# Kernel tuning notes

Hardware: AMD Instinct MI355X
Metric: run time of the kernel (lower is better)

The kernel has to match this reference:

```python
import jax, jax.numpy as jnp
import numpy as np

B, RES, NS, W, S = 2, 64, 24, 256, 256
IN_VIEW = W + 3


def setup_inputs() -> dict:
    key = jax.random.key(0)
    ks = iter(jax.random.split(key, 32))
    u = lambda k, shape, a: jax.random.uniform(k, shape, jnp.float32, -a, a)
    c_hid = float(np.sqrt(6.0 / W) / 25.0)      # SIREN hidden init bound
    c_view = float(np.sqrt(6.0 / IN_VIEW) / 25.0)
    inp = {}
    # camera: identity rotation, camera at z=1 looking down -z (StyleSDF-like)
    pose = np.zeros((B, 3, 4), np.float32)
    pose[:, 0, 0] = 1.0; pose[:, 1, 1] = 1.0; pose[:, 2, 2] = 1.0; pose[:, 2, 3] = 1.0
    inp['cam_poses'] = jnp.asarray(pose)
    inp['focal'] = jnp.full((B, 1, 1), 87.0, jnp.float32)
    inp['near'] = jnp.full((B, 1, 1), 0.88, jnp.float32)
    inp['far'] = jnp.full((B, 1, 1), 1.12, jnp.float32)
    inp['styles'] = jax.random.normal(next(ks), (B, S), jnp.float32)
    # FiLM-SIREN point layers
    inp['w0'] = u(next(ks), (W, 3), 1.0 / 3.0)
    inp['b0'] = u(next(ks), (W,), float(np.sqrt(1.0 / 3.0)))
    inp['ws'] = u(next(ks), (7, W, W), c_hid)
    inp['bs'] = u(next(ks), (7, W), float(np.sqrt(1.0 / W)))
    inp['gamma_w'] = 0.02 * jax.random.normal(next(ks), (8, W, S), jnp.float32)
    inp['gamma_b'] = u(next(ks), (8, W), float(np.sqrt(1.0 / S)))
    inp['beta_w'] = 0.02 * jax.random.normal(next(ks), (8, W, S), jnp.float32)
    inp['beta_b'] = u(next(ks), (8, W), float(np.sqrt(1.0 / S)))
    # view-conditioned FiLM layer
    inp['view_w'] = u(next(ks), (W, IN_VIEW), c_view)
    inp['view_b'] = u(next(ks), (W,), float(np.sqrt(1.0 / IN_VIEW)))
    inp['view_gw'] = 0.02 * jax.random.normal(next(ks), (W, S), jnp.float32)
    inp['view_gb'] = u(next(ks), (W,), float(np.sqrt(1.0 / S)))
    inp['view_bw'] = 0.02 * jax.random.normal(next(ks), (W, S), jnp.float32)
    inp['view_bb'] = u(next(ks), (W,), float(np.sqrt(1.0 / S)))
    # output heads (freq_init)
    inp['rgb_w'] = u(next(ks), (3, W), c_hid)
    inp['rgb_b'] = u(next(ks), (3,), float(np.sqrt(1.0 / W)))
    inp['sigma_w'] = u(next(ks), (1, W), c_hid)
    inp['sigma_b'] = u(next(ks), (1,), float(np.sqrt(1.0 / W)))
    inp['sigmoid_beta'] = 0.1 * jnp.ones((1,), jnp.float32)
    return inp


def _film(x, style, w, b, gw, gb, bw, bb):
    # x: [B,h,w,n,in] ; FiLM-SIREN: sin(gamma * (xW^T + b) + beta)
    out = jnp.einsum('bhwni,oi->bhwno', x, w) + b
    gamma = 15.0 * (style @ gw.T + gb) + 30.0          # LinearLayer(std=15, bias_init=30)
    beta = 0.25 * (style @ bw.T + bb)                  # LinearLayer(std=0.25, bias_init=0)
    return jnp.sin(gamma[:, None, None, None, :] * out + beta[:, None, None, None, :])


def _forward(cam_poses, focal, near, far, styles, w0, b0, ws, bs, gamma_w, gamma_b,
             beta_w, beta_b, view_w, view_b, view_gw, view_gb, view_bw, view_bb,
             rgb_w, rgb_b, sigma_w, sigma_b, sigmoid_beta):
    b = cam_poses.shape[0]
    # --- get_rays (buffers i, j from meshgrid, transposed) ---
    lin = jnp.linspace(0.5, RES - 0.5, RES)
    ii = jnp.broadcast_to(lin[None, :], (RES, RES))[None]  # varies along width
    jj = jnp.broadcast_to(lin[:, None], (RES, RES))[None]  # varies along height
    dirs = jnp.stack([
        jnp.broadcast_to((ii - RES * 0.5) / focal, (b, RES, RES)),
        jnp.broadcast_to(-(jj - RES * 0.5) / focal, (b, RES, RES)),
        -jnp.ones((b, RES, RES), focal.dtype)], -1)        # [B,h,w,3]
    rays_d = jnp.einsum('bhwc,bkc->bhwk', dirs, cam_poses[:, :3, :3])
    rays_o = jnp.broadcast_to(cam_poses[:, None, None, :3, -1], rays_d.shape)
    viewdirs = rays_d / jnp.linalg.norm(rays_d, axis=-1, keepdims=True)
    # --- render_rays (test: perturb=0) ---
    near4 = near[..., None] * jnp.ones_like(rays_d[..., :1])   # [B,h,w,1]
    far4 = far[..., None] * jnp.ones_like(rays_d[..., :1])
    t_vals = jnp.linspace(0.0, 1.0 - 1.0 / NS, NS)             # offset_sampling
    z_vals = near4 * (1.0 - t_vals) + far4 * t_vals            # [B,h,w,NS]
    pts = rays_o[..., None, :] + rays_d[..., None, :] * z_vals[..., None]  # [B,h,w,NS,3]
    norm_pts = pts * (2.0 / (far4 - near4))[..., None, :]      # z_normalize
    # --- SirenGenerator (styles.ndim==2 path, no hyper deltas) ---
    h = _film(norm_pts, styles, w0, b0, gamma_w[0], gamma_b[0], beta_w[0], beta_b[0])
    for i in range(7):
        h = _film(h, styles, ws[i], bs[i], gamma_w[i + 1], gamma_b[i + 1],
                  beta_w[i + 1], beta_b[i + 1])
    sdf = jnp.einsum('bhwni,oi->bhwno', h, sigma_w) + sigma_b  # [B,h,w,NS,1]
    dirs_exp = jnp.broadcast_to(viewdirs[..., None, :], pts.shape)
    h = jnp.concatenate([h, dirs_exp], -1)                     # [B,h,w,NS,W+3]
    feat = _film(h, styles, view_w, view_b, view_gw, view_gb, view_bw, view_bb)
    rgb = jnp.einsum('bhwni,oi->bhwno', feat, rgb_w) + rgb_b   # [B,h,w,NS,3]
    # --- volume_integration (with_sdf, test: no noise) ---
    rays_d_norm = jnp.linalg.norm(rays_d, axis=-1, keepdims=True)        # [B,h,w,1]
    dists = jnp.concatenate([z_vals[..., 1:] - z_vals[..., :-1],
                             jnp.full_like(rays_d_norm, 1e10)], -1)      # [B,h,w,NS]
    dists = dists * rays_d_norm
    sigma = jax.nn.sigmoid(-sdf / sigmoid_beta) / sigmoid_beta
    alpha = 1.0 - jnp.exp(-sigma * dists[..., None])                      # [B,h,w,NS,1]
    ones = jnp.ones_like(alpha[..., :1, :])
    vis = jnp.cumprod(jnp.concatenate([ones, 1.0 - alpha + 1e-10], 3), 3)[..., :-1, :]
    weights = alpha * vis
    # force_background: last sample absorbs the remaining transmittance
    bg = 1.0 - jnp.sum(weights[..., :-1, :], axis=3)
    weights = jnp.concatenate([weights[..., :-1, :], bg[..., None, :]], 3)
    rgb_map = -1.0 + 2.0 * jnp.sum(weights * jax.nn.sigmoid(rgb), axis=3)  # [B,h,w,3]
    feature_map = jnp.sum(weights * feat, axis=3)                          # [B,h,w,W]
    return jnp.concatenate([rgb_map, feature_map], -1)                     # [B,h,w,3+W]


def reference(cam_poses, focal, near, far, styles, w0, b0, ws, bs, gamma_w, gamma_b,
              beta_w, beta_b, view_w, view_b, view_gw, view_gb, view_bw, view_bb,
              rgb_w, rgb_b, sigma_w, sigma_b, sigmoid_beta):
    return _forward(cam_poses, focal, near, far, styles, w0, b0, ws, bs, gamma_w,
                    gamma_b, beta_w, beta_b, view_w, view_b, view_gw, view_gb,
                    view_bw, view_bb, rgb_w, rgb_b, sigma_w, sigma_b, sigmoid_beta)
```

## Files before the change

### kernel.cpp

```cpp
#include <hip/hip_runtime.h>
#include <hip/hip_bf16.h>

#define RESN 64
#define NS 24
#define WD 256
#define SD 256
#define NB 2
#define RPB 4
#define MP 96
#define NTH 512
#define NBLK 2048

typedef unsigned short u16;
typedef unsigned int u32;
typedef __attribute__((ext_vector_type(8))) short short8v;
typedef __attribute__((ext_vector_type(16))) float f32x16;

__device__ __forceinline__ float sigm(float x){ return 1.0f / (1.0f + expf(-x)); }

__device__ __forceinline__ float fast_sin(float x){
  float k = __builtin_rintf(x * 0.31830988618f);
  float y = fmaf(k, -3.14159274101f, x);
  y = fmaf(k, 8.74227766e-8f, y);
  float y2 = y * y;
  float p = fmaf(y2, 2.75573192e-6f, -1.98412698e-4f);
  p = fmaf(y2, p, 8.33333333e-3f);
  p = fmaf(y2, p, -1.66666667e-1f);
  float s = fmaf(y * y2, p, y);
  u32 sg = ((u32)((int)k) & 1u) << 31;
  return __uint_as_float(__float_as_uint(s) ^ sg);
}

__global__ void prep_kernel(const float* wsp, const float* vw, u16* Whi, u16* Wlo){
  int i0 = (blockIdx.x * 256 + threadIdx.x) * 4;
  #pragma unroll
  for (int j = 0; j < 4; j++){
    int e = i0 + j;
    int lay = e >> 16;
    int rk = e & 65535;
    float w = (lay < 7) ? wsp[lay * 65536 + rk]
                        : vw[(size_t)(rk >> 8) * 259 + (rk & 255)];
    u32 b = __float_as_uint(w);
    u16 hi = (u16)(b >> 16);
    float lof = w - __uint_as_float(b & 0xFFFF0000u);
    Whi[e] = hi;
    Wlo[e] = (u16)(__float_as_uint(lof) >> 16);
  }
}

__global__ void film_kernel(const float* styles, const float* gw8, const float* gb8,
                            const float* bw8, const float* bb8,
                            const float* vgw, const float* vgb, const float* vbw, const float* vbb,
                            float* G, float* Bt){
  int l = blockIdx.x >> 1, b = blockIdx.x & 1, o = threadIdx.x;
  __shared__ float st[SD];
  st[o] = styles[b * SD + o];
  __syncthreads();
  const float *gw, *bw; float gbv, bbv;
  if (l < 8){
    gw = gw8 + ((size_t)l * WD + o) * SD; bw = bw8 + ((size_t)l * WD + o) * SD;
    gbv = gb8[l * WD + o];                bbv = bb8[l * WD + o];
  } else {
    gw = vgw + (size_t)o * SD;            bw = vbw + (size_t)o * SD;
    gbv = vgb[o];                         bbv = vbb[o];
  }
  float ag = 0.f, ab = 0.f;
  for (int s = 0; s < SD; s += 2){
    ag += st[s] * gw[s] + st[s+1] * gw[s+1];
    ab += st[s] * bw[s] + st[s+1] * bw[s+1];
  }
  int idx = (l * NB + b) * WD + o;
  G[idx]  = 15.0f * (ag + gbv) + 30.0f;
  Bt[idx] = 0.25f * (ab + bbv);
}

#define SETW(LAY) { wph = Whi + (((size_t)(LAY) * WD + col) * WD) + khalf * 8;   \
                    wpl = Wlo + (((size_t)(LAY) * WD + col) * WD) + khalf * 8; }

#define PREF4 { _Pragma("unroll")                                                \
  for (int i = 0; i < 4; i++){                                                   \
    pbh[i] = *(const short8v*)(wph + i * 16);                                    \
    pbl[i] = *(const short8v*)(wpl + i * 16); } }

#define KMAIN                                                                    \
  _Pragma("unroll")                                                              \
  for (int ks = 0; ks < 16; ks++){                                               \
    short8v bh = pbh[ks & 3], bl = pbl[ks & 3];                                  \
    if (ks < 12){ pbh[ks & 3] = *(const short8v*)(wph + (ks + 4) * 16);          \
                  pbl[ks & 3] = *(const short8v*)(wpl + (ks + 4) * 16); }        \
    int ce = 2 * ks + khalf;                                                     \
    _Pragma("unroll")                                                            \
    for (int mt = 0; mt < 3; mt++){                                              \
      int elem = (mt * 32 + lane31) * WD + ((ce ^ l7) * 8);                      \
      short8v ah = *(const short8v*)(&Hhi[elem]);                                \
      short8v al = *(const short8v*)(&Hlo[elem]);                                \
      acc[mt] = __builtin_amdgcn_mfma_f32_32x32x16_bf16(ah, bh, acc[mt], 0,0,0); \
      acc[mt] = __builtin_amdgcn_mfma_f32_32x32x16_bf16(al, bh, acc[mt], 0,0,0); \
      acc[mt] = __builtin_amdgcn_mfma_f32_32x32x16_bf16(ah, bl, acc[mt], 0,0,0); \
    } }

__launch_bounds__(NTH, 2)
__global__ void render_mfma(
    const float* pose, const float* focal, const float* nearv, const float* farv,
    const float* w0, const float* b0, const float* bsp,
    const float* vw, const float* vb,
    const float* rgbw, const float* rgbb, const float* sgw, const float* sgb,
    const float* sbeta, const float* G, const float* Bt,
    const u16* Whi, const u16* Wlo, float* out)
{
  __shared__ u16 Hhi[MP * WD];
  __shared__ u16 Hlo[MP * WD];
  __shared__ float xl[MP][4];
  __shared__ float vd[RPB][4];
  __shared__ float dn[RPB];
  __shared__ float sdfl[MP];
  __shared__ float rgbl[MP][4];
  __shared__ float wtl[RPB][NS];
  __shared__ float swl[WD];
  __shared__ float rwl[3][WD];

  const int t      = threadIdx.x;
  const int lane   = t & 63;
  const int wv     = t >> 6;
  const int lane31 = lane & 31;
  const int khalf  = lane >> 5;
  const int l7     = lane31 & 7;
  const int col    = wv * 32 + lane31;
  const int om     = t & 127;
  const int mg     = t >> 7;
  const int o0     = om * 2, o1 = om * 2 + 1;
  const int mb     = mg * NS;
  const int ray0   = blockIdx.x * RPB;
  const int bidx   = ray0 >> 12;

  const u16 *wph, *wpl;
  short8v pbh[4], pbl[4];
  SETW(0); PREF4;

  if (t < WD) swl[t] = sgw[t];
  for (int i = t; i < 3 * WD; i += NTH) ((float*)rwl)[i] = rgbw[i];

  if (t < MP){
    int m = t, s = m % NS, rl = m / NS;
    int ray = ray0 + rl;
    int ww = ray & (RESN - 1);
    int hh = (ray >> 6) & (RESN - 1);
    float f = focal[bidx], nr = nearv[bidx], fr = farv[bidx];
    float di = ((ww + 0.5f) - RESN * 0.5f) / f;
    float dj = -(((hh + 0.5f) - RESN * 0.5f) / f);
    const float* P = pose + bidx * 12;
    float rdx = di * P[0] + dj * P[1] - P[2];
    float rdy = di * P[4] + dj * P[5] - P[6];
    float rdz = di * P[8] + dj * P[9] - P[10];
    float ox = P[3], oy = P[7], oz = P[11];
    float nrm = sqrtf(rdx * rdx + rdy * rdy + rdz * rdz);
    const float C = (1.0f - 1.0f / NS) / (NS - 1);
    float tv = s * C;
    float z = nr * (1.0f - tv) + fr * tv;
    float sc = 2.0f / (fr - nr);
    xl[m][0] = (ox + rdx * z) * sc;
    xl[m][1] = (oy + rdy * z) * sc;
    xl[m][2] = (oz + rdz * z) * sc;
    if (s == 0){
      vd[rl][0] = rdx / nrm; vd[rl][1] = rdy / nrm; vd[rl][2] = rdz / nrm;
      dn[rl] = nrm;
    }
  }
  __syncthreads();

  {
    float wa[3], wbv[3];
    #pragma unroll
    for (int j = 0; j < 3; j++){ wa[j] = w0[o0 * 3 + j]; wbv[j] = w0[o1 * 3 + j]; }
    float bi0 = b0[o0], bi1 = b0[o1];
    float g0 = G[bidx * WD + o0],  g1 = G[bidx * WD + o1];
    float e0 = Bt[bidx * WD + o0], e1 = Bt[bidx * WD + o1];
    #pragma unroll
    for (int m = 0; m < NS; m++){
      int row = mb + m;
      float x0 = xl[row][0], x1 = xl[row][1], x2 = xl[row][2];
      float u0 = x0 * wa[0]  + x1 * wa[1]  + x2 * wa[2]  + bi0;
      float u1 = x0 * wbv[0] + x1 * wbv[1] + x2 * wbv[2] + bi1;
      float s0 = fast_sin(fmaf(g0, u0, e0));
      float s1 = fast_sin(fmaf(g1, u1, e1));
      u32 bs0 = __float_as_uint(s0), bs1 = __float_as_uint(s1);
      u32 hw = (bs0 >> 16) | (bs1 & 0xFFFF0000u);
      float l0f = s0 - __uint_as_float(bs0 & 0xFFFF0000u);
      float l1f = s1 - __uint_as_float(bs1 & 0xFFFF0000u);
      u32 lw = (__float_as_uint(l0f) >> 16) | (__float_as_uint(l1f) & 0xFFFF0000u);
      int eidx = row * WD + (((o0 >> 3) ^ (row & 7)) * 8) + (o0 & 7);
      *(u32*)&Hhi[eidx] = hw;
      *(u32*)&Hlo[eidx] = lw;
    }
  }
  __syncthreads();

  #pragma unroll 1
  for (int l = 0; l < 7; l++){
    f32x16 acc[3];
    #pragma unroll
    for (int mt = 0; mt < 3; mt++)
      #pragma unroll
      for (int j = 0; j < 16; j++) acc[mt][j] = 0.f;
    KMAIN
    float g  = G[((l + 1) * NB + bidx) * WD + col];
    float e  = Bt[((l + 1) * NB + bidx) * WD + col];
    float bi = bsp[l * WD + col];
    __syncthreads();
    #pragma unroll
    for (int mt = 0; mt < 3; mt++){
      #pragma unroll
      for (int rg = 0; rg < 16; rg++){
        int row = mt * 32 + (rg & 3) + 8 * (rg >> 2) + 4 * khalf;
        float a = acc[mt][rg] + bi;
        float s = fast_sin(fmaf(g, a, e));
        u32 sb = __float_as_uint(s);
        int eidx = row * WD + ((((col >> 3) ^ (row & 7))) * 8) + (col & 7);
        Hhi[eidx] = (u16)(sb >> 16);
        float sl = s - __uint_as_float(sb & 0xFFFF0000u);
        Hlo[eidx] = (u16)(__float_as_uint(sl) >> 16);
      }
    }
    SETW(l + 1); PREF4;
    __syncthreads();
  }

  f32x16 acc[3];
  #pragma unroll
  for (int mt = 0; mt < 3; mt++)
    #pragma unroll
    for (int j = 0; j < 16; j++) acc[mt][j] = 0.f;
  KMAIN
  float vt0 = vw[(size_t)col * 259 + 256];
  float vt1 = vw[(size_t)col * 259 + 257];
  float vt2 = vw[(size_t)col * 259 + 258];
  float vbv = vb[col];
  float gv = G[(8 * NB + bidx) * WD + col];
  float ev = Bt[(8 * NB + bidx) * WD + col];

  if (t < MP){
    float a = 0.f;
    #pragma unroll 4
    for (int c = 0; c < 32; c++){
      int eb = t * WD + ((c ^ (t & 7)) * 8);
      short8v hv = *(const short8v*)(&Hhi[eb]);
      short8v lv = *(const short8v*)(&Hlo[eb]);
      #pragma unroll
      for (int j = 0; j < 8; j++){
        float h = __uint_as_float(((u32)(u16)hv[j]) << 16)
                + __uint_as_float(((u32)(u16)lv[j]) << 16);
        a = fmaf(h, swl[c * 8 + j], a);
      }
    }
    sdfl[t] = a + sgb[0];
  }
  __syncthreads();

  #pragma unroll
  for (int mt = 0; mt < 3; mt++){
    #pragma unroll
    for (int rg = 0; rg < 16; rg++){
      int row = mt * 32 + (rg & 3) + 8 * (rg >> 2) + 4 * khalf;
      int ray = (row >= 48) ? ((row >= 72) ? 3 : 2) : ((row >= 24) ? 1 : 0);
      float c = vd[ray][0] * vt0 + vd[ray][1] * vt1 + vd[ray][2] * vt2 + vbv;
      float a = acc[mt][rg] + c;
      float s = fast_sin(fmaf(gv, a, ev));
      u32 sb = __float_as_uint(s);
      int eidx = row * WD + ((((col >> 3) ^ (row & 7))) * 8) + (col & 7);
      Hhi[eidx] = (u16)(sb >> 16);
      float sl = s - __uint_as_float(sb & 0xFFFF0000u);
      Hlo[eidx] = (u16)(__float_as_uint(sl) >> 16);
    }
  }
  __syncthreads();

  if (t < MP){
    float a0 = 0.f, a1 = 0.f, a2 = 0.f;
    #pragma unroll 4
    for (int c = 0; c < 32; c++){
      int eb = t * WD + ((c ^ (t & 7)) * 8);
      short8v hv = *(const short8v*)(&Hhi[eb]);
      short8v lv = *(const short8v*)(&Hlo[eb]);
      #pragma unroll
      for (int j = 0; j < 8; j++){
        float h = __uint_as_float(((u32)(u16)hv[j]) << 16)
                + __uint_as_float(((u32)(u16)lv[j]) << 16);
        int k = c * 8 + j;
        a0 = fmaf(h, rwl[0][k], a0);
        a1 = fmaf(h, rwl[1][k], a1);
        a2 = fmaf(h, rwl[2][k], a2);
      }
    }
    rgbl[t][0] = a0 + rgbb[0];
    rgbl[t][1] = a1 + rgbb[1];
    rgbl[t][2] = a2 + rgbb[2];
  }
  __syncthreads();

  if (t < RPB){
    int r = t;
    int ray = ray0 + r;
    float nr = nearv[bidx], fr = farv[bidx];
    float dnv = dn[r];
    float bet = sbeta[0];
    float vis = 1.f, wsum = 0.f, cr = 0.f, cg = 0.f, cb = 0.f;
    const float C = (1.0f - 1.0f / NS) / (NS - 1);
    #pragma unroll
    for (int s = 0; s < NS; s++){
      float w;
      if (s < NS - 1){
        float t0v = s * C, t1v = (s + 1) * C;
        float z0 = nr * (1.f - t0v) + fr * t0v;
        float z1 = nr * (1.f - t1v) + fr * t1v;
        float dist = (z1 - z0) * dnv;
        float sg = sigm(-sdfl[r * NS + s] / bet) / bet;
        float al = 1.f - expf(-sg * dist);
        w = al * vis;
        vis *= (1.f - al + 1e-10f);
        wsum += w;
      } else {
        w = 1.f - wsum;
      }
      wtl[r][s] = w;
      cr += w * sigm(rgbl[r * NS + s][0]);
      cg += w * sigm(rgbl[r * NS + s][1]);
      cb += w * sigm(rgbl[r * NS + s][2]);
    }
    size_t ob = (size_t)ray * 259;
    out[ob + 0] = -1.f + 2.f * cr;
    out[ob + 1] = -1.f + 2.f * cg;
    out[ob + 2] = -1.f + 2.f * cb;
  }
  __syncthreads();

  {
    float f0 = 0.f, f1 = 0.f;
    #pragma unroll
    for (int s = 0; s < NS; s++){
      int row = mb + s;
      float w = wtl[mg][s];
      int eidx = row * WD + (((o0 >> 3) ^ (row & 7)) * 8) + (o0 & 7);
      u32 wh = *(const u32*)&Hhi[eidx];
      u32 wl = *(const u32*)&Hlo[eidx];
      float fa = __uint_as_float(wh << 16) + __uint_as_float(wl << 16);
      float fb = __uint_as_float(wh & 0xFFFF0000u) + __uint_as_float(wl & 0xFFFF0000u);
      f0 = fmaf(w, fa, f0);
      f1 = fmaf(w, fb, f1);
    }
    size_t ob = (size_t)(ray0 + mg) * 259 + 3;
    out[ob + o0] = f0;
    out[ob + o1] = f1;
  }
}

extern "C" void kernel_launch(void* const* d_in, const int* in_sizes, int n_in,
                              void* d_out, int out_size, void* d_ws, size_t ws_size,
                              hipStream_t stream) {
  (void)in_sizes; (void)n_in; (void)out_size;
  const float* pose   = (const float*)d_in[0];
  const float* focal  = (const float*)d_in[1];
  const float* nearv  = (const float*)d_in[2];
  const float* farv   = (const float*)d_in[3];
  const float* styles = (const float*)d_in[4];
  const float* w0     = (const float*)d_in[5];
  const float* b0     = (const float*)d_in[6];
  const float* wsp    = (const float*)d_in[7];
  const float* bsp    = (const float*)d_in[8];
  const float* gw8    = (const float*)d_in[9];
  const float* gb8    = (const float*)d_in[10];
  const float* bw8    = (const float*)d_in[11];
  const float* bb8    = (const float*)d_in[12];
  const float* vw     = (const float*)d_in[13];
  const float* vb     = (const float*)d_in[14];
  const float* vgw    = (const float*)d_in[15];
  const float* vgb    = (const float*)d_in[16];
  const float* vbw    = (const float*)d_in[17];
  const float* vbb    = (const float*)d_in[18];
  const float* rgbw   = (const float*)d_in[19];
  const float* rgbb   = (const float*)d_in[20];
  const float* sgw    = (const float*)d_in[21];
  const float* sgb    = (const float*)d_in[22];
  const float* sbeta  = (const float*)d_in[23];

  float* G  = (float*)d_ws;
  float* Bt = G + 9 * NB * WD;
  float* out = (float*)d_out;

  const size_t plane_off = 36864;
  const size_t plane_elems = (size_t)8 * WD * WD;

  u16* Whi = (u16*)((char*)d_ws + plane_off);
  u16* Wlo = Whi + plane_elems;

  film_kernel<<<dim3(18), dim3(256), 0, stream>>>(styles, gw8, gb8, bw8, bb8,
                                                  vgw, vgb, vbw, vbb, G, Bt);
  prep_kernel<<<dim3(512), dim3(256), 0, stream>>>(wsp, vw, Whi, Wlo);
  render_mfma<<<dim3(NBLK), dim3(NTH), 0, stream>>>(pose, focal, nearv, farv,
      w0, b0, bsp, vw, vb, rgbw, rgbb, sgw, sgb, sbeta, G, Bt, Whi, Wlo, out);
}
```

Measured before the change: 844.2 us.

## Halve rays per block and switch to 16x16x32 MFMA tiles with 4 waves

Each block now handles 2 rays (48 sample rows) with 256 threads instead of 4 rays with 512 threads, doubling the grid. The GEMM moves from 32x32x16 MFMA with a prefetched weight ring to 16x16x32 MFMA, where each wave covers 64 output columns over 3x4 tiles and loads weights directly per k-step. Shared staging of the sigma and rgb head weights is dropped in favour of global reads, and the first layer and feature-map loops are recast as one column per thread. This aims for higher occupancy (launch bounds 3) and smaller LDS per block, but each block now re-reads the full weight set for half as many rows, doubling global and L2 weight traffic.

```diff
diff --git a/kernel.cpp b/kernel.cpp
--- a/kernel.cpp
+++ b/kernel.cpp
@@ -6,15 +6,15 @@
 #define WD 256
 #define SD 256
 #define NB 2
-#define RPB 4
-#define MP 96
-#define NTH 512
-#define NBLK 2048
+#define RPB 2
+#define MP 48
+#define NTH 256
+#define NBLK 4096
 
 typedef unsigned short u16;
 typedef unsigned int u32;
 typedef __attribute__((ext_vector_type(8))) short short8v;
-typedef __attribute__((ext_vector_type(16))) float f32x16;
+typedef __attribute__((ext_vector_type(4))) float f32x4;
 
 __device__ __forceinline__ float sigm(float x){ return 1.0f / (1.0f + expf(-x)); }
 
@@ -74,32 +74,31 @@
   Bt[idx] = 0.25f * (ab + bbv);
 }
 
-#define SETW(LAY) { wph = Whi + (((size_t)(LAY) * WD + col) * WD) + khalf * 8;   \
-                    wpl = Wlo + (((size_t)(LAY) * WD + col) * WD) + khalf * 8; }
-
-#define PREF4 { _Pragma("unroll")                                                \
-  for (int i = 0; i < 4; i++){                                                   \
-    pbh[i] = *(const short8v*)(wph + i * 16);                                    \
-    pbl[i] = *(const short8v*)(wpl + i * 16); } }
-
-#define KMAIN                                                                    \
-  _Pragma("unroll")                                                              \
-  for (int ks = 0; ks < 16; ks++){                                               \
-    short8v bh = pbh[ks & 3], bl = pbl[ks & 3];                                  \
-    if (ks < 12){ pbh[ks & 3] = *(const short8v*)(wph + (ks + 4) * 16);          \
-                  pbl[ks & 3] = *(const short8v*)(wpl + (ks + 4) * 16); }        \
-    int ce = 2 * ks + khalf;                                                     \
-    _Pragma("unroll")                                                            \
-    for (int mt = 0; mt < 3; mt++){                                              \
-      int elem = (mt * 32 + lane31) * WD + ((ce ^ l7) * 8);                      \
-      short8v ah = *(const short8v*)(&Hhi[elem]);                                \
-      short8v al = *(const short8v*)(&Hlo[elem]);                                \
-      acc[mt] = __builtin_amdgcn_mfma_f32_32x32x16_bf16(ah, bh, acc[mt], 0,0,0); \
-      acc[mt] = __builtin_amdgcn_mfma_f32_32x32x16_bf16(al, bh, acc[mt], 0,0,0); \
-      acc[mt] = __builtin_amdgcn_mfma_f32_32x32x16_bf16(ah, bl, acc[mt], 0,0,0); \
-    } }
-
-__launch_bounds__(NTH, 2)
+#define KMAIN16(LAY)                                                              \
+{ const u16* wbh = Whi + (((size_t)(LAY) * WD + wv * 64 + l15) * WD) + lk * 8;    \
+  const u16* wbl = Wlo + (((size_t)(LAY) * WD + wv * 64 + l15) * WD) + lk * 8;    \
+  _Pragma("unroll 2")                                                             \
+  for (int ks = 0; ks < 8; ks++){                                                 \
+    short8v bh[4], bl[4];                                                         \
+    _Pragma("unroll")                                                             \
+    for (int nt = 0; nt < 4; nt++){                                               \
+      bh[nt] = *(const short8v*)(wbh + nt * 4096 + ks * 32);                      \
+      bl[nt] = *(const short8v*)(wbl + nt * 4096 + ks * 32);                      \
+    }                                                                             \
+    int ac = ((ks * 4 + lk) ^ l7) * 8;                                            \
+    _Pragma("unroll")                                                             \
+    for (int mt = 0; mt < 3; mt++){                                               \
+      int ar = (mt * 16 + l15) * WD + ac;                                         \
+      short8v ah = *(const short8v*)(&Hhi[ar]);                                   \
+      short8v al = *(const short8v*)(&Hlo[ar]);                                   \
+      _Pragma("unroll")                                                           \
+      for (int nt = 0; nt < 4; nt++){                                             \
+        acc[mt][nt] = __builtin_amdgcn_mfma_f32_16x16x32_bf16(ah, bh[nt], acc[mt][nt], 0,0,0); \
+        acc[mt][nt] = __builtin_amdgcn_mfma_f32_16x16x32_bf16(al, bh[nt], acc[mt][nt], 0,0,0); \
+        acc[mt][nt] = __builtin_amdgcn_mfma_f32_16x16x32_bf16(ah, bl[nt], acc[mt][nt], 0,0,0); \
+      } } } }
+
+__launch_bounds__(NTH, 3)
 __global__ void render_mfma(
     const float* pose, const float* focal, const float* nearv, const float* farv,
     const float* w0, const float* b0, const float* bsp,
@@ -116,29 +115,15 @@
   __shared__ float sdfl[MP];
   __shared__ float rgbl[MP][4];
   __shared__ float wtl[RPB][NS];
-  __shared__ float swl[WD];
-  __shared__ float rwl[3][WD];
-
-  const int t      = threadIdx.x;
-  const int lane   = t & 63;
-  const int wv     = t >> 6;
-  const int lane31 = lane & 31;
-  const int khalf  = lane >> 5;
-  const int l7     = lane31 & 7;
-  const int col    = wv * 32 + lane31;
-  const int om     = t & 127;
-  const int mg     = t >> 7;
-  const int o0     = om * 2, o1 = om * 2 + 1;
-  const int mb     = mg * NS;
-  const int ray0   = blockIdx.x * RPB;
-  const int bidx   = ray0 >> 12;
-
-  const u16 *wph, *wpl;
-  short8v pbh[4], pbl[4];
-  SETW(0); PREF4;
-
-  if (t < WD) swl[t] = sgw[t];
-  for (int i = t; i < 3 * WD; i += NTH) ((float*)rwl)[i] = rgbw[i];
+
+  const int t    = threadIdx.x;
+  const int lane = t & 63;
+  const int wv   = t >> 6;
+  const int l15  = lane & 15;
+  const int lk   = lane >> 4;
+  const int l7   = l15 & 7;
+  const int ray0 = blockIdx.x * RPB;
+  const int bidx = ray0 >> 12;
 
   if (t < MP){
     int m = t, s = m % NS, rl = m / NS;
@@ -169,116 +154,134 @@
   __syncthreads();
 
   {
-    float wa[3], wbv[3];
-    #pragma unroll
-    for (int j = 0; j < 3; j++){ wa[j] = w0[o0 * 3 + j]; wbv[j] = w0[o1 * 3 + j]; }
-    float bi0 = b0[o0], bi1 = b0[o1];
-    float g0 = G[bidx * WD + o0],  g1 = G[bidx * WD + o1];
-    float e0 = Bt[bidx * WD + o0], e1 = Bt[bidx * WD + o1];
-    #pragma unroll
-    for (int m = 0; m < NS; m++){
-      int row = mb + m;
-      float x0 = xl[row][0], x1 = xl[row][1], x2 = xl[row][2];
-      float u0 = x0 * wa[0]  + x1 * wa[1]  + x2 * wa[2]  + bi0;
-      float u1 = x0 * wbv[0] + x1 * wbv[1] + x2 * wbv[2] + bi1;
-      float s0 = fast_sin(fmaf(g0, u0, e0));
-      float s1 = fast_sin(fmaf(g1, u1, e1));
-      u32 bs0 = __float_as_uint(s0), bs1 = __float_as_uint(s1);
-      u32 hw = (bs0 >> 16) | (bs1 & 0xFFFF0000u);
-      float l0f = s0 - __uint_as_float(bs0 & 0xFFFF0000u);
-      float l1f = s1 - __uint_as_float(bs1 & 0xFFFF0000u);
-      u32 lw = (__float_as_uint(l0f) >> 16) | (__float_as_uint(l1f) & 0xFFFF0000u);
-      int eidx = row * WD + (((o0 >> 3) ^ (row & 7)) * 8) + (o0 & 7);
-      *(u32*)&Hhi[eidx] = hw;
-      *(u32*)&Hlo[eidx] = lw;
+    int c = t;
+    float wa0 = w0[c * 3], wa1 = w0[c * 3 + 1], wa2 = w0[c * 3 + 2];
+    float bi = b0[c];
+    float g = G[bidx * WD + c], e = Bt[bidx * WD + c];
+    int chi = c >> 3;
+    #pragma unroll 4
+    for (int m = 0; m < MP; m++){
+      float u = xl[m][0] * wa0 + xl[m][1] * wa1 + xl[m][2] * wa2 + bi;
+      float s = fast_sin(fmaf(g, u, e));
+      u32 sb = __float_as_uint(s);
+      int eidx = m * WD + ((chi ^ (m & 7)) * 8) + (c & 7);
+      Hhi[eidx] = (u16)(sb >> 16);
+      float sl = s - __uint_as_float(sb & 0xFFFF0000u);
+      Hlo[eidx] = (u16)(__float_as_uint(sl) >> 16);
     }
   }
   __syncthreads();
 
   #pragma unroll 1
   for (int l = 0; l < 7; l++){
-    f32x16 acc[3];
+    f32x4 acc[3][4];
     #pragma unroll
     for (int mt = 0; mt < 3; mt++)
       #pragma unroll
-      for (int j = 0; j < 16; j++) acc[mt][j] = 0.f;
-    KMAIN
-    float g  = G[((l + 1) * NB + bidx) * WD + col];
-    float e  = Bt[((l + 1) * NB + bidx) * WD + col];
-    float bi = bsp[l * WD + col];
+      for (int nt = 0; nt < 4; nt++)
+        #pragma unroll
+        for (int j = 0; j < 4; j++) acc[mt][nt][j] = 0.f;
+    KMAIN16(l)
+    int gi = (l + 1) * NB + bidx;
+    float gv[4], ev[4], bv[4];
+    #pragma unroll
+    for (int nt = 0; nt < 4; nt++){
+      int c = wv * 64 + nt * 16 + l15;
+      gv[nt] = G[gi * WD + c];
+      ev[nt] = Bt[gi * WD + c];
+      bv[nt] = bsp[l * WD + c];
+    }
     __syncthreads();
     #pragma unroll
+    for (int nt = 0; nt < 4; nt++){
+      int chi = wv * 8 + nt * 2 + (l15 >> 3);
+      #pragma unroll
+      for (int mt = 0; mt < 3; mt++){
+        #pragma unroll
+        for (int rg = 0; rg < 4; rg++){
+          int row = mt * 16 + lk * 4 + rg;
+          float a = acc[mt][nt][rg] + bv[nt];
+          float s = fast_sin(fmaf(gv[nt], a, ev[nt]));
+          u32 sb = __float_as_uint(s);
+          int eidx = row * WD + ((chi ^ (row & 7)) * 8) + l7;
+          Hhi[eidx] = (u16)(sb >> 16);
+          float sl = s - __uint_as_float(sb & 0xFFFF0000u);
+          Hlo[eidx] = (u16)(__float_as_uint(sl) >> 16);
+        }
+      }
+    }
+    __syncthreads();
+  }
+
+  f32x4 acc[3][4];
+  #pragma unroll
+  for (int mt = 0; mt < 3; mt++)
+    #pragma unroll
+    for (int nt = 0; nt < 4; nt++)
+      #pragma unroll
+      for (int j = 0; j < 4; j++) acc[mt][nt][j] = 0.f;
+  KMAIN16(7)
+  float vt0[4], vt1[4], vt2[4], vbv[4], gvv[4], evv[4];
+  #pragma unroll
+  for (int nt = 0; nt < 4; nt++){
+    int c = wv * 64 + nt * 16 + l15;
+    vt0[nt] = vw[(size_t)c * 259 + 256];
+    vt1[nt] = vw[(size_t)c * 259 + 257];
+    vt2[nt] = vw[(size_t)c * 259 + 258];
+    vbv[nt] = vb[c];
+    gvv[nt] = G[(8 * NB + bidx) * WD + c];
+    evv[nt] = Bt[(8 * NB + bidx) * WD + c];
+  }
+
+  if (t < MP){
+    float a = 0.f;
+    int t7 = t & 7;
+    #pragma unroll 4
+    for (int c = 0; c < 32; c++){
+      int eb = t * WD + ((c ^ t7) * 8);
+      short8v hv = *(const short8v*)(&Hhi[eb]);
+      short8v lv = *(const short8v*)(&Hlo[eb]);
+      #pragma unroll
+      for (int j = 0; j < 8; j++){
+        float h = __uint_as_float(((u32)(u16)hv[j]) << 16)
+                + __uint_as_float(((u32)(u16)lv[j]) << 16);
+        a = fmaf(h, sgw[c * 8 + j], a);
+      }
+    }
+    sdfl[t] = a + sgb[0];
+  }
+  __syncthreads();
+
+  #pragma unroll
+  for (int nt = 0; nt < 4; nt++){
+    int chi = wv * 8 + nt * 2 + (l15 >> 3);
+    #pragma unroll
     for (int mt = 0; mt < 3; mt++){
       #pragma unroll
-      for (int rg = 0; rg < 16; rg++){
-        int row = mt * 32 + (rg & 3) + 8 * (rg >> 2) + 4 * khalf;
-        float a = acc[mt][rg] + bi;
-        float s = fast_sin(fmaf(g, a, e));
+      for (int rg = 0; rg < 4; rg++){
+        int row = mt * 16 + lk * 4 + rg;
+        int ray = row >= NS ? 1 : 0;
+        float c = vd[ray][0] * vt0[nt] + vd[ray][1] * vt1[nt]
+                + vd[ray][2] * vt2[nt] + vbv[nt];
+        float a = acc[mt][nt][rg] + c;
+        float s = fast_sin(fmaf(gvv[nt], a, evv[nt]));
         u32 sb = __float_as_uint(s);
-        int eidx = row * WD + ((((col >> 3) ^ (row & 7))) * 8) + (col & 7);
+        int eidx = row * WD + ((chi ^ (row & 7)) * 8) + l7;
         Hhi[eidx] = (u16)(sb >> 16);
         float sl = s - __uint_as_float(sb & 0xFFFF0000u);
         Hlo[eidx] = (u16)(__float_as_uint(sl) >> 16);
       }
     }
-    SETW(l + 1); PREF4;
-    __syncthreads();
-  }
-
-  f32x16 acc[3];
-  #pragma unroll
-  for (int mt = 0; mt < 3; mt++)
-    #pragma unroll
-    for (int j = 0; j < 16; j++) acc[mt][j] = 0.f;
-  KMAIN
-  float vt0 = vw[(size_t)col * 259 + 256];
-  float vt1 = vw[(size_t)col * 259 + 257];
-  float vt2 = vw[(size_t)col * 259 + 258];
-  float vbv = vb[col];
-  float gv = G[(8 * NB + bidx) * WD + col];
-  float ev = Bt[(8 * NB + bidx) * WD + col];
-
-  if (t < MP){
-    float a = 0.f;
-    #pragma unroll 4
-    for (int c = 0; c < 32; c++){
-      int eb = t * WD + ((c ^ (t & 7)) * 8);
-      short8v hv = *(const short8v*)(&Hhi[eb]);
-      short8v lv = *(const short8v*)(&Hlo[eb]);
-      #pragma unroll
-      for (int j = 0; j < 8; j++){
-        float h = __uint_as_float(((u32)(u16)hv[j]) << 16)
-                + __uint_as_float(((u32)(u16)lv[j]) << 16);
-        a = fmaf(h, swl[c * 8 + j], a);
-      }
-    }
-    sdfl[t] = a + sgb[0];
-  }
-  __syncthreads();
-
-  #pragma unroll
-  for (int mt = 0; mt < 3; mt++){
-    #pragma unroll
-    for (int rg = 0; rg < 16; rg++){
-      int row = mt * 32 + (rg & 3) + 8 * (rg >> 2) + 4 * khalf;
-      int ray = (row >= 48) ? ((row >= 72) ? 3 : 2) : ((row >= 24) ? 1 : 0);
-      float c = vd[ray][0] * vt0 + vd[ray][1] * vt1 + vd[ray][2] * vt2 + vbv;
-      float a = acc[mt][rg] + c;
-      float s = fast_sin(fmaf(gv, a, ev));
-      u32 sb = __float_as_uint(s);
-      int eidx = row * WD + ((((col >> 3) ^ (row & 7))) * 8) + (col & 7);
-      Hhi[eidx] = (u16)(sb >> 16);
-      float sl = s - __uint_as_float(sb & 0xFFFF0000u);
-      Hlo[eidx] = (u16)(__float_as_uint(sl) >> 16);
-    }
-  }
-  __syncthreads();
-
-  if (t < MP){
+  }
+  __syncthreads();
+
+  if (t >= 64 && t < 64 + MP){
+    int r = t - 64;
+    int r7 = r & 7;
     float a0 = 0.f, a1 = 0.f, a2 = 0.f;
     #pragma unroll 4
     for (int c = 0; c < 32; c++){
-      int eb = t * WD + ((c ^ (t & 7)) * 8);
+      int eb = r * WD + ((c ^ r7) * 8);
       short8v hv = *(const short8v*)(&Hhi[eb]);
       short8v lv = *(const short8v*)(&Hlo[eb]);
       #pragma unroll
@@ -286,14 +289,14 @@
         float h = __uint_as_float(((u32)(u16)hv[j]) << 16)
                 + __uint_as_float(((u32)(u16)lv[j]) << 16);
         int k = c * 8 + j;
-        a0 = fmaf(h, rwl[0][k], a0);
-        a1 = fmaf(h, rwl[1][k], a1);
-        a2 = fmaf(h, rwl[2][k], a2);
-      }
-    }
-    rgbl[t][0] = a0 + rgbb[0];
-    rgbl[t][1] = a1 + rgbb[1];
-    rgbl[t][2] = a2 + rgbb[2];
+        a0 = fmaf(h, rgbw[k], a0);
+        a1 = fmaf(h, rgbw[WD + k], a1);
+        a2 = fmaf(h, rgbw[2 * WD + k], a2);
+      }
+    }
+    rgbl[r][0] = a0 + rgbb[0];
+    rgbl[r][1] = a1 + rgbb[1];
+    rgbl[r][2] = a2 + rgbb[2];
   }
   __syncthreads();
 
@@ -334,29 +337,28 @@
   __syncthreads();
 
   {
-    float f0 = 0.f, f1 = 0.f;
-    #pragma unroll
-    for (int s = 0; s < NS; s++){
-      int row = mb + s;
-      float w = wtl[mg][s];
-      int eidx = row * WD + (((o0 >> 3) ^ (row & 7)) * 8) + (o0 & 7);
-      u32 wh = *(const u32*)&Hhi[eidx];
-      u32 wl = *(const u32*)&Hlo[eidx];
-      float fa = __uint_as_float(wh << 16) + __uint_as_float(wl << 16);
-      float fb = __uint_as_float(wh & 0xFFFF0000u) + __uint_as_float(wl & 0xFFFF0000u);
-      f0 = fmaf(w, fa, f0);
-      f1 = fmaf(w, fb, f1);
-    }
-    size_t ob = (size_t)(ray0 + mg) * 259 + 3;
-    out[ob + o0] = f0;
-    out[ob + o1] = f1;
+    int c = t;
+    int chi = c >> 3, cl = c & 7;
+    #pragma unroll
+    for (int r = 0; r < RPB; r++){
+      float fa = 0.f;
+      #pragma unroll 4
+      for (int s = 0; s < NS; s++){
+        int row = r * NS + s;
+        int eidx = row * WD + ((chi ^ (row & 7)) * 8) + cl;
+        float h = __uint_as_float(((u32)Hhi[eidx]) << 16)
+                + __uint_as_float(((u32)Hlo[eidx]) << 16);
+        fa = fmaf(wtl[r][s], h, fa);
+      }
+      out[(size_t)(ray0 + r) * 259 + 3 + c] = fa;
+    }
   }
 }
 
 extern "C" void kernel_launch(void* const* d_in, const int* in_sizes, int n_in,
                               void* d_out, int out_size, void* d_ws, size_t ws_size,
                               hipStream_t stream) {
-  (void)in_sizes; (void)n_in; (void)out_size;
+  (void)in_sizes; (void)n_in; (void)out_size; (void)ws_size;
   const float* pose   = (const float*)d_in[0];
   const float* focal  = (const float*)d_in[1];
   const float* nearv  = (const float*)d_in[2];
```

Result: slower. 1.197 ms (+41.8%).

## Swap MFMA operands to transpose accumulator layout and vectorize epilogue LDS stores

Applied to the files above, without the earlier changes.

The A and B operands of the bf16 MFMA are swapped, so each lane's accumulator registers now hold consecutive output columns for a single row instead of scattered rows. The epilogues of the hidden and view layers are rewritten to match: per-column FiLM parameters are loaded as float4, and each thread packs four bf16 hi/lo values into 64-bit LDS stores instead of issuing sixteen scalar 16-bit stores per tile. The aim is to cut LDS store instructions and scalar global loads in the epilogue. It depends on the output mapping and the swizzled slot indexing being exactly right for the transposed layout.

```diff
diff --git a/kernel.cpp b/kernel.cpp
--- a/kernel.cpp
+++ b/kernel.cpp
@@ -94,9 +94,9 @@
       int elem = (mt * 32 + lane31) * WD + ((ce ^ l7) * 8);                      \
       short8v ah = *(const short8v*)(&Hhi[elem]);                                \
       short8v al = *(const short8v*)(&Hlo[elem]);                                \
-      acc[mt] = __builtin_amdgcn_mfma_f32_32x32x16_bf16(ah, bh, acc[mt], 0,0,0); \
-      acc[mt] = __builtin_amdgcn_mfma_f32_32x32x16_bf16(al, bh, acc[mt], 0,0,0); \
-      acc[mt] = __builtin_amdgcn_mfma_f32_32x32x16_bf16(ah, bl, acc[mt], 0,0,0); \
+      acc[mt] = __builtin_amdgcn_mfma_f32_32x32x16_bf16(bh, ah, acc[mt], 0,0,0); \
+      acc[mt] = __builtin_amdgcn_mfma_f32_32x32x16_bf16(bh, al, acc[mt], 0,0,0); \
+      acc[mt] = __builtin_amdgcn_mfma_f32_32x32x16_bf16(bl, ah, acc[mt], 0,0,0); \
     } }
 
 __launch_bounds__(NTH, 2)
@@ -203,22 +203,33 @@
       #pragma unroll
       for (int j = 0; j < 16; j++) acc[mt][j] = 0.f;
     KMAIN
-    float g  = G[((l + 1) * NB + bidx) * WD + col];
-    float e  = Bt[((l + 1) * NB + bidx) * WD + col];
-    float bi = bsp[l * WD + col];
+    int gi = (l + 1) * NB + bidx;
     __syncthreads();
     #pragma unroll
-    for (int mt = 0; mt < 3; mt++){
-      #pragma unroll
-      for (int rg = 0; rg < 16; rg++){
-        int row = mt * 32 + (rg & 3) + 8 * (rg >> 2) + 4 * khalf;
-        float a = acc[mt][rg] + bi;
-        float s = fast_sin(fmaf(g, a, e));
-        u32 sb = __float_as_uint(s);
-        int eidx = row * WD + ((((col >> 3) ^ (row & 7))) * 8) + (col & 7);
-        Hhi[eidx] = (u16)(sb >> 16);
-        float sl = s - __uint_as_float(sb & 0xFFFF0000u);
-        Hlo[eidx] = (u16)(__float_as_uint(sl) >> 16);
+    for (int q = 0; q < 4; q++){
+      int cq = wv * 32 + q * 8 + khalf * 4;
+      float4 g4 = *(const float4*)&G[gi * WD + cq];
+      float4 e4 = *(const float4*)&Bt[gi * WD + cq];
+      float4 b4 = *(const float4*)&bsp[l * WD + cq];
+      int slotc = (wv * 4 + q);
+      #pragma unroll
+      for (int mt = 0; mt < 3; mt++){
+        int row = mt * 32 + lane31;
+        u32 hp[4], lp[4];
+        #pragma unroll
+        for (int i = 0; i < 4; i++){
+          float a = acc[mt][q * 4 + i] + b4[i];
+          float s = fast_sin(fmaf(g4[i], a, e4[i]));
+          u32 sb = __float_as_uint(s);
+          hp[i] = sb >> 16;
+          float sl = s - __uint_as_float(sb & 0xFFFF0000u);
+          lp[i] = __float_as_uint(sl) >> 16;
+        }
+        int idx = row * WD + ((slotc ^ (row & 7)) * 8) + khalf * 4;
+        uint2 H; H.x = hp[0] | (hp[1] << 16); H.y = hp[2] | (hp[3] << 16);
+        uint2 L; L.x = lp[0] | (lp[1] << 16); L.y = lp[2] | (lp[3] << 16);
+        *(uint2*)&Hhi[idx] = H;
+        *(uint2*)&Hlo[idx] = L;
       }
     }
     SETW(l + 1); PREF4;
@@ -231,12 +242,6 @@
     #pragma unroll
     for (int j = 0; j < 16; j++) acc[mt][j] = 0.f;
   KMAIN
-  float vt0 = vw[(size_t)col * 259 + 256];
-  float vt1 = vw[(size_t)col * 259 + 257];
-  float vt2 = vw[(size_t)col * 259 + 258];
-  float vbv = vb[col];
-  float gv = G[(8 * NB + bidx) * WD + col];
-  float ev = Bt[(8 * NB + bidx) * WD + col];
 
   if (t < MP){
     float a = 0.f;
@@ -256,20 +261,43 @@
   }
   __syncthreads();
 
-  #pragma unroll
-  for (int mt = 0; mt < 3; mt++){
-    #pragma unroll
-    for (int rg = 0; rg < 16; rg++){
-      int row = mt * 32 + (rg & 3) + 8 * (rg >> 2) + 4 * khalf;
-      int ray = (row >= 48) ? ((row >= 72) ? 3 : 2) : ((row >= 24) ? 1 : 0);
-      float c = vd[ray][0] * vt0 + vd[ray][1] * vt1 + vd[ray][2] * vt2 + vbv;
-      float a = acc[mt][rg] + c;
-      float s = fast_sin(fmaf(gv, a, ev));
-      u32 sb = __float_as_uint(s);
-      int eidx = row * WD + ((((col >> 3) ^ (row & 7))) * 8) + (col & 7);
-      Hhi[eidx] = (u16)(sb >> 16);
-      float sl = s - __uint_as_float(sb & 0xFFFF0000u);
-      Hlo[eidx] = (u16)(__float_as_uint(sl) >> 16);
+  {
+    int gi8 = (8 * NB + bidx) * WD;
+    #pragma unroll
+    for (int q = 0; q < 4; q++){
+      int cq = wv * 32 + q * 8 + khalf * 4;
+      float t0q[4], t1q[4], t2q[4];
+      #pragma unroll
+      for (int i = 0; i < 4; i++){
+        const float* vr = vw + (size_t)(cq + i) * 259;
+        t0q[i] = vr[256]; t1q[i] = vr[257]; t2q[i] = vr[258];
+      }
+      float4 vb4 = *(const float4*)&vb[cq];
+      float4 g4  = *(const float4*)&G[gi8 + cq];
+      float4 e4  = *(const float4*)&Bt[gi8 + cq];
+      int slotc = (wv * 4 + q);
+      #pragma unroll
+      for (int mt = 0; mt < 3; mt++){
+        int row = mt * 32 + lane31;
+        int rayi = (row >= 48) ? ((row >= 72) ? 3 : 2) : ((row >= 24) ? 1 : 0);
+        float d0 = vd[rayi][0], d1 = vd[rayi][1], d2 = vd[rayi][2];
+        u32 hp[4], lp[4];
+        #pragma unroll
+        for (int i = 0; i < 4; i++){
+          float c = d0 * t0q[i] + d1 * t1q[i] + d2 * t2q[i] + vb4[i];
+          float a = acc[mt][q * 4 + i] + c;
+          float s = fast_sin(fmaf(g4[i], a, e4[i]));
+          u32 sb = __float_as_uint(s);
+          hp[i] = sb >> 16;
+          float sl = s - __uint_as_float(sb & 0xFFFF0000u);
+          lp[i] = __float_as_uint(sl) >> 16;
+        }
+        int idx = row * WD + ((slotc ^ (row & 7)) * 8) + khalf * 4;
+        uint2 H; H.x = hp[0] | (hp[1] << 16); H.y = hp[2] | (hp[3] << 16);
+        uint2 L; L.x = lp[0] | (lp[1] << 16); L.y = lp[2] | (lp[3] << 16);
+        *(uint2*)&Hhi[idx] = H;
+        *(uint2*)&Hlo[idx] = L;
+      }
     }
   }
   __syncthreads();
@@ -356,7 +384,7 @@
 extern "C" void kernel_launch(void* const* d_in, const int* in_sizes, int n_in,
                               void* d_out, int out_size, void* d_ws, size_t ws_size,
                               hipStream_t stream) {
-  (void)in_sizes; (void)n_in; (void)out_size;
+  (void)in_sizes; (void)n_in; (void)out_size; (void)ws_size;
   const float* pose   = (const float*)d_in[0];
   const float* focal  = (const float*)d_in[1];
   const float* nearv  = (const float*)d_in[2];
```

New measurement: 869.8 us. +3.0%, slower.

## Halve rays per block to two, padding MFMA rows to 64 for higher occupancy

Applied to the files above, without the earlier changes.

Each block now handles two rays (48 sample rows), padded to 64 rows with zeroed LDS so the MFMA loop uses two 32-row tiles instead of three. The block count doubles and launch bounds ask for four blocks per CU, aiming at more occupancy and less per-block register and LDS pressure. The sigma and rgb head weights are now read directly from global memory instead of being staged in LDS. The first layer and feature reduction move from two columns per thread to one. The cost is a third of the MFMA work wasted on padding rows (64 computed for 48 used versus 96 for 96) and weight fetches amortized over fewer rays.

```diff
diff --git a/kernel.cpp b/kernel.cpp
--- a/kernel.cpp
+++ b/kernel.cpp
@@ -6,10 +6,11 @@
 #define WD 256
 #define SD 256
 #define NB 2
-#define RPB 4
-#define MP 96
+#define RPB 2
+#define MP 48
+#define MPA 64
 #define NTH 512
-#define NBLK 2048
+#define NBLK 4096
 
 typedef unsigned short u16;
 typedef unsigned int u32;
@@ -90,7 +91,7 @@
                   pbl[ks & 3] = *(const short8v*)(wpl + (ks + 4) * 16); }        \
     int ce = 2 * ks + khalf;                                                     \
     _Pragma("unroll")                                                            \
-    for (int mt = 0; mt < 3; mt++){                                              \
+    for (int mt = 0; mt < 2; mt++){                                              \
       int elem = (mt * 32 + lane31) * WD + ((ce ^ l7) * 8);                      \
       short8v ah = *(const short8v*)(&Hhi[elem]);                                \
       short8v al = *(const short8v*)(&Hlo[elem]);                                \
@@ -99,7 +100,7 @@
       acc[mt] = __builtin_amdgcn_mfma_f32_32x32x16_bf16(ah, bl, acc[mt], 0,0,0); \
     } }
 
-__launch_bounds__(NTH, 2)
+__launch_bounds__(NTH, 4)
 __global__ void render_mfma(
     const float* pose, const float* focal, const float* nearv, const float* farv,
     const float* w0, const float* b0, const float* bsp,
@@ -108,16 +109,14 @@
     const float* sbeta, const float* G, const float* Bt,
     const u16* Whi, const u16* Wlo, float* out)
 {
-  __shared__ u16 Hhi[MP * WD];
-  __shared__ u16 Hlo[MP * WD];
+  __shared__ u16 Hhi[MPA * WD];
+  __shared__ u16 Hlo[MPA * WD];
   __shared__ float xl[MP][4];
   __shared__ float vd[RPB][4];
   __shared__ float dn[RPB];
   __shared__ float sdfl[MP];
   __shared__ float rgbl[MP][4];
   __shared__ float wtl[RPB][NS];
-  __shared__ float swl[WD];
-  __shared__ float rwl[3][WD];
 
   const int t      = threadIdx.x;
   const int lane   = t & 63;
@@ -126,10 +125,8 @@
   const int khalf  = lane >> 5;
   const int l7     = lane31 & 7;
   const int col    = wv * 32 + lane31;
-  const int om     = t & 127;
-  const int mg     = t >> 7;
-  const int o0     = om * 2, o1 = om * 2 + 1;
-  const int mb     = mg * NS;
+  const int cidx   = t & 255;
+  const int rg2    = t >> 8;
   const int ray0   = blockIdx.x * RPB;
   const int bidx   = ray0 >> 12;
 
@@ -137,8 +134,11 @@
   short8v pbh[4], pbl[4];
   SETW(0); PREF4;
 
-  if (t < WD) swl[t] = sgw[t];
-  for (int i = t; i < 3 * WD; i += NTH) ((float*)rwl)[i] = rgbw[i];
+  {
+    u32* zh = (u32*)&Hhi[MP * WD];
+    u32* zl = (u32*)&Hlo[MP * WD];
+    for (int i = t; i < ((MPA - MP) * WD) / 2; i += NTH){ zh[i] = 0u; zl[i] = 0u; }
+  }
 
   if (t < MP){
     int m = t, s = m % NS, rl = m / NS;
@@ -169,46 +169,40 @@
   __syncthreads();
 
   {
-    float wa[3], wbv[3];
-    #pragma unroll
-    for (int j = 0; j < 3; j++){ wa[j] = w0[o0 * 3 + j]; wbv[j] = w0[o1 * 3 + j]; }
-    float bi0 = b0[o0], bi1 = b0[o1];
-    float g0 = G[bidx * WD + o0],  g1 = G[bidx * WD + o1];
-    float e0 = Bt[bidx * WD + o0], e1 = Bt[bidx * WD + o1];
+    int c = cidx;
+    float wa0 = w0[c * 3], wa1 = w0[c * 3 + 1], wa2 = w0[c * 3 + 2];
+    float bi = b0[c];
+    float g = G[bidx * WD + c], e = Bt[bidx * WD + c];
+    int chi = c >> 3, cl = c & 7;
     #pragma unroll
     for (int m = 0; m < NS; m++){
-      int row = mb + m;
-      float x0 = xl[row][0], x1 = xl[row][1], x2 = xl[row][2];
-      float u0 = x0 * wa[0]  + x1 * wa[1]  + x2 * wa[2]  + bi0;
-      float u1 = x0 * wbv[0] + x1 * wbv[1] + x2 * wbv[2] + bi1;
-      float s0 = fast_sin(fmaf(g0, u0, e0));
-      float s1 = fast_sin(fmaf(g1, u1, e1));
-      u32 bs0 = __float_as_uint(s0), bs1 = __float_as_uint(s1);
-      u32 hw = (bs0 >> 16) | (bs1 & 0xFFFF0000u);
-      float l0f = s0 - __uint_as_float(bs0 & 0xFFFF0000u);
-      float l1f = s1 - __uint_as_float(bs1 & 0xFFFF0000u);
-      u32 lw = (__float_as_uint(l0f) >> 16) | (__float_as_uint(l1f) & 0xFFFF0000u);
-      int eidx = row * WD + (((o0 >> 3) ^ (row & 7)) * 8) + (o0 & 7);
-      *(u32*)&Hhi[eidx] = hw;
-      *(u32*)&Hlo[eidx] = lw;
+      int row = rg2 * NS + m;
+      float u = xl[row][0] * wa0 + xl[row][1] * wa1 + xl[row][2] * wa2 + bi;
+      float s = fast_sin(fmaf(g, u, e));
+      u32 sb = __float_as_uint(s);
+      int eidx = row * WD + ((chi ^ (row & 7)) * 8) + cl;
+      Hhi[eidx] = (u16)(sb >> 16);
+      float sl = s - __uint_as_float(sb & 0xFFFF0000u);
+      Hlo[eidx] = (u16)(__float_as_uint(sl) >> 16);
     }
   }
   __syncthreads();
 
   #pragma unroll 1
   for (int l = 0; l < 7; l++){
-    f32x16 acc[3];
-    #pragma unroll
-    for (int mt = 0; mt < 3; mt++)
+    f32x16 acc[2];
+    #pragma unroll
+    for (int mt = 0; mt < 2; mt++)
       #pragma unroll
       for (int j = 0; j < 16; j++) acc[mt][j] = 0.f;
     KMAIN
-    float g  = G[((l + 1) * NB + bidx) * WD + col];
-    float e  = Bt[((l + 1) * NB + bidx) * WD + col];
+    int gi = (l + 1) * NB + bidx;
+    float g  = G[gi * WD + col];
+    float e  = Bt[gi * WD + col];
     float bi = bsp[l * WD + col];
     __syncthreads();
     #pragma unroll
-    for (int mt = 0; mt < 3; mt++){
+    for (int mt = 0; mt < 2; mt++){
       #pragma unroll
       for (int rg = 0; rg < 16; rg++){
         int row = mt * 32 + (rg & 3) + 8 * (rg >> 2) + 4 * khalf;
@@ -225,9 +219,9 @@
     __syncthreads();
   }
 
-  f32x16 acc[3];
+  f32x16 acc[2];
   #pragma unroll
-  for (int mt = 0; mt < 3; mt++)
+  for (int mt = 0; mt < 2; mt++)
     #pragma unroll
     for (int j = 0; j < 16; j++) acc[mt][j] = 0.f;
   KMAIN
@@ -249,7 +243,7 @@
       for (int j = 0; j < 8; j++){
         float h = __uint_as_float(((u32)(u16)hv[j]) << 16)
                 + __uint_as_float(((u32)(u16)lv[j]) << 16);
-        a = fmaf(h, swl[c * 8 + j], a);
+        a = fmaf(h, sgw[c * 8 + j], a);
       }
     }
     sdfl[t] = a + sgb[0];
@@ -257,12 +251,12 @@
   __syncthreads();
 
   #pragma unroll
-  for (int mt = 0; mt < 3; mt++){
+  for (int mt = 0; mt < 2; mt++){
     #pragma unroll
     for (int rg = 0; rg < 16; rg++){
       int row = mt * 32 + (rg & 3) + 8 * (rg >> 2) + 4 * khalf;
-      int ray = (row >= 48) ? ((row >= 72) ? 3 : 2) : ((row >= 24) ? 1 : 0);
-      float c = vd[ray][0] * vt0 + vd[ray][1] * vt1 + vd[ray][2] * vt2 + vbv;
+      int rayi = (row >= NS) ? 1 : 0;
+      float c = vd[rayi][0] * vt0 + vd[rayi][1] * vt1 + vd[rayi][2] * vt2 + vbv;
       float a = acc[mt][rg] + c;
       float s = fast_sin(fmaf(gv, a, ev));
       u32 sb = __float_as_uint(s);
@@ -286,9 +280,9 @@
         float h = __uint_as_float(((u32)(u16)hv[j]) << 16)
                 + __uint_as_float(((u32)(u16)lv[j]) << 16);
         int k = c * 8 + j;
-        a0 = fmaf(h, rwl[0][k], a0);
-        a1 = fmaf(h, rwl[1][k], a1);
-        a2 = fmaf(h, rwl[2][k], a2);
+        a0 = fmaf(h, rgbw[k], a0);
+        a1 = fmaf(h, rgbw[WD + k], a1);
+        a2 = fmaf(h, rgbw[2 * WD + k], a2);
       }
     }
     rgbl[t][0] = a0 + rgbb[0];
@@ -334,29 +328,25 @@
   __syncthreads();
 
   {
-    float f0 = 0.f, f1 = 0.f;
-    #pragma unroll
+    int c = cidx;
+    int chi = c >> 3, cl = c & 7;
+    float fa = 0.f;
+    #pragma unroll 4
     for (int s = 0; s < NS; s++){
-      int row = mb + s;
-      float w = wtl[mg][s];
-      int eidx = row * WD + (((o0 >> 3) ^ (row & 7)) * 8) + (o0 & 7);
-      u32 wh = *(const u32*)&Hhi[eidx];
-      u32 wl = *(const u32*)&Hlo[eidx];
-      float fa = __uint_as_float(wh << 16) + __uint_as_float(wl << 16);
-      float fb = __uint_as_float(wh & 0xFFFF0000u) + __uint_as_float(wl & 0xFFFF0000u);
-      f0 = fmaf(w, fa, f0);
-      f1 = fmaf(w, fb, f1);
-    }
-    size_t ob = (size_t)(ray0 + mg) * 259 + 3;
-    out[ob + o0] = f0;
-    out[ob + o1] = f1;
+      int row = rg2 * NS + s;
+      int eidx = row * WD + ((chi ^ (row & 7)) * 8) + cl;
+      float h = __uint_as_float(((u32)Hhi[eidx]) << 16)
+              + __uint_as_float(((u32)Hlo[eidx]) << 16);
+      fa = fmaf(wtl[rg2][s], h, fa);
+    }
+    out[(size_t)(ray0 + rg2) * 259 + 3 + c] = fa;
   }
 }
 
 extern "C" void kernel_launch(void* const* d_in, const int* in_sizes, int n_in,
                               void* d_out, int out_size, void* d_ws, size_t ws_size,
                               hipStream_t stream) {
-  (void)in_sizes; (void)n_in; (void)out_size;
+  (void)in_sizes; (void)n_in; (void)out_size; (void)ws_size;
   const float* pose   = (const float*)d_in[0];
   const float* focal  = (const float*)d_in[1];
   const float* nearv  = (const float*)d_in[2];
```

Result: slower. 1.381 ms (+63.6%).
